# Kernel tuning notes

Hardware: AMD Instinct MI355X
Metric: run time of the kernel (lower is better)

Reference implementation:

```python
import jax, jax.numpy as jnp
import numpy as np

N_NODES = 100000
N_EDGES = 1600000
IN_CH = 64
OUT_CH = 64
EDGE_DIM = 32


def setup_inputs() -> dict:
    key = jax.random.key(0)
    ks = jax.random.split(key, 8)
    cat_dim = 2 * IN_CH + EDGE_DIM  # 160
    x = jax.random.normal(ks[0], (N_NODES, IN_CH), dtype=jnp.float32)
    edge_index = jax.random.randint(ks[1], (2, N_EDGES), 0, N_NODES, dtype=jnp.int64)
    edge_attr = jax.random.normal(ks[2], (N_EDGES, EDGE_DIM), dtype=jnp.float32)
    # linear1: (2*in + edge_dim) -> out ; stored as [in, out] for x @ W
    W1 = jax.random.normal(ks[3], (cat_dim, OUT_CH), dtype=jnp.float32) / np.sqrt(cat_dim)
    b1 = jnp.zeros((OUT_CH,), dtype=jnp.float32)
    gamma = jnp.ones((OUT_CH,), dtype=jnp.float32)
    beta = jnp.zeros((OUT_CH,), dtype=jnp.float32)
    W2 = jax.random.normal(ks[4], (OUT_CH, OUT_CH), dtype=jnp.float32) / np.sqrt(OUT_CH)
    b2 = jnp.zeros((OUT_CH,), dtype=jnp.float32)
    return {"x": x, "edge_index": edge_index, "edge_attr": edge_attr,
            "W1": W1, "b1": b1, "gamma": gamma, "beta": beta, "W2": W2, "b2": b2}


def _layer_norm(h, gamma, beta, eps=1e-5):
    mu = jnp.mean(h, axis=-1, keepdims=True)
    var = jnp.var(h, axis=-1, keepdims=True)
    return (h - mu) * jax.lax.rsqrt(var + eps) * gamma + beta


def reference(x, edge_index, edge_attr, W1, b1, gamma, beta, W2, b2):
    i, j = edge_index[0], edge_index[1]
    # gather source/target node features and concat with edge features: [E, 2*in+edge_dim]
    feats = jnp.concatenate([x[i], x[j], edge_attr], axis=-1)
    h = feats @ W1 + b1                       # [E, out]
    h = jax.nn.gelu(_layer_norm(h, gamma, beta), approximate=False)
    m = h @ W2 + b2                           # [E, out]
    # scatter-add messages onto target nodes j, dim_size = N
    return jax.ops.segment_sum(m, j, num_segments=x.shape[0])
```

## Files before the change

kernel.cpp:

```cpp
#include <hip/hip_runtime.h>
#include <math.h>


using short8 = __attribute__((ext_vector_type(8))) short;
using f32x4  = __attribute__((ext_vector_type(4))) float;

#define LDH 72

static __device__ __forceinline__ short f2bf(float f) {
    unsigned u = __float_as_uint(f);
    u += 0x7FFFu + ((u >> 16) & 1u);
    return (short)(u >> 16);
}

static __device__ __forceinline__ short8 pack8(float4 a, float4 b) {
    short8 r;
    r[0] = f2bf(a.x); r[1] = f2bf(a.y); r[2] = f2bf(a.z); r[3] = f2bf(a.w);
    r[4] = f2bf(b.x); r[5] = f2bf(b.y); r[6] = f2bf(b.z); r[7] = f2bf(b.w);
    return r;
}

__global__ __launch_bounds__(256) void prep_all(
    const float* __restrict__ x,
    const float* __restrict__ W1,
    const float* __restrict__ W2,
    short* __restrict__ Wt1,
    short* __restrict__ Wt2,
    short* __restrict__ xbf,
    float* __restrict__ out,
    int N, int out_elems, int doX)
{
    const int tid = blockIdx.x * 256 + threadIdx.x;
    const int TT  = gridDim.x * 256;

    const int nf4 = out_elems >> 2;
    const float4 z = make_float4(0.f, 0.f, 0.f, 0.f);
    for (int i = tid; i < nf4; i += TT) ((float4*)out)[i] = z;
    for (int i = (nf4 << 2) + tid; i < out_elems; i += TT) out[i] = 0.f;

    for (int t = tid; t < 160 * 64; t += TT) {
        int k = t / 64, n = t % 64;
        Wt1[n * 160 + k] = f2bf(W1[t]);
    }
    for (int t = tid; t < 64 * 64; t += TT) {
        int k = t / 64, n = t % 64;
        Wt2[n * 64 + k] = f2bf(W2[t]);
    }
    if (doX) {
        const float4* xf4 = (const float4*)x;
        for (int t = tid; t < N * 8; t += TT) {
            float4 a = xf4[2 * t];
            float4 b = xf4[2 * t + 1];
            ((short8*)xbf)[t] = pack8(a, b);
        }
    }
}

template <bool XBF>
__global__ __launch_bounds__(256) void mpconv_mfma(
    const float* __restrict__ x,
    const short* __restrict__ xbf,
    const int*   __restrict__ ei,
    const float* __restrict__ ea,
    const short* __restrict__ Wt1,
    const float* __restrict__ b1,
    const float* __restrict__ gam,
    const float* __restrict__ bet,
    const short* __restrict__ Wt2,
    const float* __restrict__ b2,
    float*       __restrict__ out,
    int E)
{
    __shared__ __align__(16) short Hlds[4][64][LDH];

    const int wave = threadIdx.x >> 6;
    const int lane = threadIdx.x & 63;
    const int g    = lane >> 4;
    const int col  = lane & 15;
    const int eb   = blockIdx.x * 256 + wave * 64;

    int aedge[4], ii[4], jj[4];
#pragma unroll
    for (int mt = 0; mt < 4; mt++) {
        int e = eb + mt * 16 + col;
        e = (e < E) ? e : (E - 1);
        aedge[mt] = e;
        ii[mt] = ei[e];
        jj[mt] = ei[E + e];
    }

    float b1c[4], gc[4], bc[4], b2c[4];
#pragma unroll
    for (int nt = 0; nt < 4; nt++) {
        int c = col + 16 * nt;
        b1c[nt] = b1[c]; gc[nt] = gam[c]; bc[nt] = bet[c]; b2c[nt] = b2[c];
    }

    f32x4 acc[4][4];
#pragma unroll
    for (int mt = 0; mt < 4; mt++)
#pragma unroll
        for (int nt = 0; nt < 4; nt++)
            acc[mt][nt] = (f32x4){0.f, 0.f, 0.f, 0.f};

#pragma unroll
    for (int ks = 0; ks < 5; ks++) {
        const int k0 = ks * 32;
        const int kk = k0 + g * 8;

        short8 afrag[4];
#pragma unroll
        for (int mt = 0; mt < 4; mt++) {
            if (XBF && k0 < 64) {
                afrag[mt] = *(const short8*)(xbf + (size_t)ii[mt] * 64 + kk);
            } else if (XBF && k0 < 128) {
                afrag[mt] = *(const short8*)(xbf + (size_t)jj[mt] * 64 + (kk - 64));
            } else {
                const float* s;
                if (k0 < 64)       s = x  + (size_t)ii[mt] * 64 + kk;
                else if (k0 < 128) s = x  + (size_t)jj[mt] * 64 + (kk - 64);
                else               s = ea + (size_t)aedge[mt] * 32 + (kk - 128);
                float4 a = *(const float4*)s;
                float4 b = *(const float4*)(s + 4);
                afrag[mt] = pack8(a, b);
            }
        }
        short8 bfrag[4];
#pragma unroll
        for (int nt = 0; nt < 4; nt++)
            bfrag[nt] = *(const short8*)(Wt1 + (size_t)(col + 16 * nt) * 160 + kk);

#pragma unroll
        for (int mt = 0; mt < 4; mt++)
#pragma unroll
            for (int nt = 0; nt < 4; nt++)
                acc[mt][nt] = __builtin_amdgcn_mfma_f32_16x16x32_bf16(
                    afrag[mt], bfrag[nt], acc[mt][nt], 0, 0, 0);
    }

#pragma unroll
    for (int mt = 0; mt < 4; mt++) {
        float s[4] = {0.f, 0.f, 0.f, 0.f};
        float q[4] = {0.f, 0.f, 0.f, 0.f};
#pragma unroll
        for (int nt = 0; nt < 4; nt++) {
#pragma unroll
            for (int r = 0; r < 4; r++) {
                float v = acc[mt][nt][r] + b1c[nt];
                acc[mt][nt][r] = v;
                s[r] += v;
                q[r] += v * v;
            }
        }
#pragma unroll
        for (int m = 1; m < 16; m <<= 1) {
#pragma unroll
            for (int r = 0; r < 4; r++) {
                s[r] += __shfl_xor(s[r], m);
                q[r] += __shfl_xor(q[r], m);
            }
        }
#pragma unroll
        for (int r = 0; r < 4; r++) {
            float mu  = s[r] * (1.0f / 64.0f);
            float var = q[r] * (1.0f / 64.0f) - mu * mu;
            float inv = rsqrtf(var + 1e-5f);
            int row = mt * 16 + g * 4 + r;
#pragma unroll
            for (int nt = 0; nt < 4; nt++) {
                float h = (acc[mt][nt][r] - mu) * inv * gc[nt] + bc[nt];
                h = 0.5f * h * (1.0f + erff(h * 0.70710678118654752f));
                Hlds[wave][row][col + 16 * nt] = f2bf(h);
            }
        }
    }
    __syncthreads();

    f32x4 acc2[4][4];
#pragma unroll
    for (int mt = 0; mt < 4; mt++)
#pragma unroll
        for (int nt = 0; nt < 4; nt++)
            acc2[mt][nt] = (f32x4){0.f, 0.f, 0.f, 0.f};

#pragma unroll
    for (int ks = 0; ks < 2; ks++) {
        const int kk = ks * 32 + g * 8;
        short8 af[4], bf[4];
#pragma unroll
        for (int mt = 0; mt < 4; mt++)
            af[mt] = *(const short8*)&Hlds[wave][mt * 16 + col][kk];
#pragma unroll
        for (int nt = 0; nt < 4; nt++)
            bf[nt] = *(const short8*)(Wt2 + (size_t)(col + 16 * nt) * 64 + kk);
#pragma unroll
        for (int mt = 0; mt < 4; mt++)
#pragma unroll
            for (int nt = 0; nt < 4; nt++)
                acc2[mt][nt] = __builtin_amdgcn_mfma_f32_16x16x32_bf16(
                    af[mt], bf[nt], acc2[mt][nt], 0, 0, 0);
    }

#pragma unroll
    for (int mt = 0; mt < 4; mt++) {
#pragma unroll
        for (int r = 0; r < 4; r++) {
            int e = eb + mt * 16 + g * 4 + r;
            if (e < E) {
                int dst = ei[E + e];
                float* op = out + (size_t)dst * 64 + col;
#pragma unroll
                for (int nt = 0; nt < 4; nt++)
                    unsafeAtomicAdd(op + 16 * nt, acc2[mt][nt][r] + b2c[nt]);
            }
        }
    }
}

extern "C" void kernel_launch(void* const* d_in, const int* in_sizes, int n_in,
                              void* d_out, int out_size, void* d_ws, size_t ws_size,
                              hipStream_t stream)
{
    const float* x   = (const float*)d_in[0];
    const int*   ei  = (const int*)  d_in[1];
    const float* ea  = (const float*)d_in[2];
    const float* W1  = (const float*)d_in[3];
    const float* b1  = (const float*)d_in[4];
    const float* gam = (const float*)d_in[5];
    const float* bet = (const float*)d_in[6];
    const float* W2  = (const float*)d_in[7];
    const float* b2  = (const float*)d_in[8];
    float* out = (float*)d_out;

    const int E = in_sizes[1] / 2;
    const int N = in_sizes[0] / 64;

    short* Wt1 = (short*)d_ws;
    short* Wt2 = Wt1 + 160 * 64;
    const size_t woff = (size_t)(160 * 64 + 64 * 64) * sizeof(short);
    short* xbf = (short*)((char*)d_ws + woff);
    const size_t need_xbf = woff + (size_t)N * 64 * sizeof(short);
    const int use_xbf = (ws_size >= need_xbf) ? 1 : 0;

    hipLaunchKernelGGL(prep_all, dim3(1024), dim3(256), 0, stream,
                       x, W1, W2, Wt1, Wt2, xbf, out, N, out_size, use_xbf);

    {
        int grid = (E + 255) / 256;
        if (use_xbf)
            hipLaunchKernelGGL(mpconv_mfma<true>, dim3(grid), dim3(256), 0, stream,
                               x, xbf, ei, ea, Wt1, b1, gam, bet, Wt2, b2, out, E);
        else
            hipLaunchKernelGGL(mpconv_mfma<false>, dim3(grid), dim3(256), 0, stream,
                               x, xbf, ei, ea, Wt1, b1, gam, bet, Wt2, b2, out, E);
    }
}
```

Measured before the change: 692.9 us.

## Sort edges by destination and pre-reduce messages per wave before atomics

Adds a counting sort of edges by destination node: a histogram, a two-level scan and a scatter that builds an (edge, src, dst) index array. The fused edge kernel then walks the sorted edges, stages each 32-row slice of the output messages in shared memory and sums runs that share a destination before issuing one atomic per run. The goal is to cut global atomic traffic and improve locality of the scatter-add. In exchange it adds four small kernels and a 16-byte-per-edge array, and reads of edge_attr and x[i] become scattered.

```diff
diff --git a/kernel.cpp b/kernel.cpp
--- a/kernel.cpp
+++ b/kernel.cpp
@@ -6,6 +6,8 @@
 using f32x4  = __attribute__((ext_vector_type(4))) float;
 
 #define LDH 72
+#define WREG 9472
+#define SMEM_BYTES (4 * WREG)
 
 static __device__ __forceinline__ short f2bf(float f) {
     unsigned u = __float_as_uint(f);
@@ -27,8 +29,9 @@
     short* __restrict__ Wt1,
     short* __restrict__ Wt2,
     short* __restrict__ xbf,
+    int*   __restrict__ counts,
     float* __restrict__ out,
-    int N, int out_elems, int doX)
+    int N, int out_elems, int doX, int doSort)
 {
     const int tid = blockIdx.x * 256 + threadIdx.x;
     const int TT  = gridDim.x * 256;
@@ -37,6 +40,9 @@
     const float4 z = make_float4(0.f, 0.f, 0.f, 0.f);
     for (int i = tid; i < nf4; i += TT) ((float4*)out)[i] = z;
     for (int i = (nf4 << 2) + tid; i < out_elems; i += TT) out[i] = 0.f;
+
+    if (doSort)
+        for (int i = tid; i < N; i += TT) counts[i] = 0;
 
     for (int t = tid; t < 160 * 64; t += TT) {
         int k = t / 64, n = t % 64;
@@ -54,6 +60,239 @@
             ((short8*)xbf)[t] = pack8(a, b);
         }
     }
+}
+
+__global__ void hist_dst(const int* __restrict__ ei, int* __restrict__ counts, int E)
+{
+    int e = blockIdx.x * blockDim.x + threadIdx.x;
+    if (e < E) atomicAdd(&counts[ei[E + e]], 1);
+}
+
+__global__ __launch_bounds__(256) void scan_local(const int* __restrict__ counts,
+                                                  int* __restrict__ offs,
+                                                  int* __restrict__ bsum, int N)
+{
+    __shared__ int sc[256];
+    const int t = threadIdx.x;
+    const int i = blockIdx.x * 256 + t;
+    int v = (i < N) ? counts[i] : 0;
+    sc[t] = v;
+    __syncthreads();
+    for (int d = 1; d < 256; d <<= 1) {
+        int u = (t >= d) ? sc[t - d] : 0;
+        __syncthreads();
+        sc[t] += u;
+        __syncthreads();
+    }
+    if (i < N) offs[i] = sc[t] - v;
+    if (t == 255) bsum[blockIdx.x] = sc[255];
+}
+
+__global__ __launch_bounds__(1024) void scan_tops(const int* __restrict__ bsum,
+                                                  int* __restrict__ boff, int nb)
+{
+    __shared__ int sc[1024];
+    const int t = threadIdx.x;
+    int v = (t < nb) ? bsum[t] : 0;
+    sc[t] = v;
+    __syncthreads();
+    for (int d = 1; d < 1024; d <<= 1) {
+        int u = (t >= d) ? sc[t - d] : 0;
+        __syncthreads();
+        sc[t] += u;
+        __syncthreads();
+    }
+    if (t < nb) boff[t] = sc[t] - v;
+}
+
+__global__ void build_etri(const int* __restrict__ ei, int* __restrict__ offs,
+                           const int* __restrict__ boff,
+                           int4* __restrict__ etri, int E)
+{
+    int e = blockIdx.x * blockDim.x + threadIdx.x;
+    if (e < E) {
+        int src = ei[e];
+        int dst = ei[E + e];
+        int pos = atomicAdd(&offs[dst], 1) + boff[dst >> 8];
+        etri[pos] = make_int4(e, src, dst, 0);
+    }
+}
+
+__global__ __launch_bounds__(256) void mpconv_sorted(
+    const short* __restrict__ xbf,
+    const float* __restrict__ ea,
+    const short* __restrict__ Wt1,
+    const float* __restrict__ b1,
+    const float* __restrict__ gam,
+    const float* __restrict__ bet,
+    const short* __restrict__ Wt2,
+    const float* __restrict__ b2,
+    const int4*  __restrict__ etri,
+    float*       __restrict__ out,
+    int E)
+{
+    __shared__ __align__(16) char smem[SMEM_BYTES];
+
+    const int wave = threadIdx.x >> 6;
+    const int lane = threadIdx.x & 63;
+    const int g    = lane >> 4;
+    const int col  = lane & 15;
+    const int eb   = blockIdx.x * 256 + wave * 64;
+
+    char* wbase = smem + wave * WREG;
+    short (*Hl)[LDH] = (short (*)[LDH])wbase;
+    float (*Hf)[66]  = (float (*)[66])wbase;
+    int*  dstL       = (int*)(wbase + 9216);
+
+    int aedge[4], ii[4], jj[4];
+#pragma unroll
+    for (int mt = 0; mt < 4; mt++) {
+        int ep = eb + mt * 16 + col;
+        bool v = (ep < E);
+        int epc = v ? ep : (E - 1);
+        int4 t4 = etri[epc];
+        aedge[mt] = t4.x;
+        ii[mt] = t4.y;
+        jj[mt] = t4.z;
+        if (g == 0) dstL[mt * 16 + col] = v ? t4.z : -1;
+    }
+
+    float b1c[4], gc[4], bc[4], b2c[4];
+#pragma unroll
+    for (int nt = 0; nt < 4; nt++) {
+        int c = col + 16 * nt;
+        b1c[nt] = b1[c]; gc[nt] = gam[c]; bc[nt] = bet[c]; b2c[nt] = b2[c];
+    }
+
+    f32x4 acc[4][4];
+#pragma unroll
+    for (int mt = 0; mt < 4; mt++)
+#pragma unroll
+        for (int nt = 0; nt < 4; nt++)
+            acc[mt][nt] = (f32x4){0.f, 0.f, 0.f, 0.f};
+
+#pragma unroll
+    for (int ks = 0; ks < 5; ks++) {
+        const int k0 = ks * 32;
+        const int kk = k0 + g * 8;
+
+        short8 afrag[4];
+#pragma unroll
+        for (int mt = 0; mt < 4; mt++) {
+            if (k0 < 64) {
+                afrag[mt] = *(const short8*)(xbf + (size_t)ii[mt] * 64 + kk);
+            } else if (k0 < 128) {
+                afrag[mt] = *(const short8*)(xbf + (size_t)jj[mt] * 64 + (kk - 64));
+            } else {
+                const float* s = ea + (size_t)aedge[mt] * 32 + (kk - 128);
+                float4 a = *(const float4*)s;
+                float4 b = *(const float4*)(s + 4);
+                afrag[mt] = pack8(a, b);
+            }
+        }
+        short8 bfrag[4];
+#pragma unroll
+        for (int nt = 0; nt < 4; nt++)
+            bfrag[nt] = *(const short8*)(Wt1 + (size_t)(col + 16 * nt) * 160 + kk);
+
+#pragma unroll
+        for (int mt = 0; mt < 4; mt++)
+#pragma unroll
+            for (int nt = 0; nt < 4; nt++)
+                acc[mt][nt] = __builtin_amdgcn_mfma_f32_16x16x32_bf16(
+                    afrag[mt], bfrag[nt], acc[mt][nt], 0, 0, 0);
+    }
+
+#pragma unroll
+    for (int mt = 0; mt < 4; mt++) {
+        float s[4] = {0.f, 0.f, 0.f, 0.f};
+        float q[4] = {0.f, 0.f, 0.f, 0.f};
+#pragma unroll
+        for (int nt = 0; nt < 4; nt++) {
+#pragma unroll
+            for (int r = 0; r < 4; r++) {
+                float v = acc[mt][nt][r] + b1c[nt];
+                acc[mt][nt][r] = v;
+                s[r] += v;
+                q[r] += v * v;
+            }
+        }
+#pragma unroll
+        for (int m = 1; m < 16; m <<= 1) {
+#pragma unroll
+            for (int r = 0; r < 4; r++) {
+                s[r] += __shfl_xor(s[r], m);
+                q[r] += __shfl_xor(q[r], m);
+            }
+        }
+#pragma unroll
+        for (int r = 0; r < 4; r++) {
+            float mu  = s[r] * (1.0f / 64.0f);
+            float var = q[r] * (1.0f / 64.0f) - mu * mu;
+            float inv = rsqrtf(var + 1e-5f);
+            int row = mt * 16 + g * 4 + r;
+#pragma unroll
+            for (int nt = 0; nt < 4; nt++) {
+                float h = (acc[mt][nt][r] - mu) * inv * gc[nt] + bc[nt];
+                h = 0.5f * h * (1.0f + erff(h * 0.70710678118654752f));
+                Hl[row][col + 16 * nt] = f2bf(h);
+            }
+        }
+    }
+
+    f32x4 acc2[4][4];
+#pragma unroll
+    for (int mt = 0; mt < 4; mt++)
+#pragma unroll
+        for (int nt = 0; nt < 4; nt++)
+            acc2[mt][nt] = (f32x4){0.f, 0.f, 0.f, 0.f};
+
+#pragma unroll
+    for (int ks = 0; ks < 2; ks++) {
+        const int kk = ks * 32 + g * 8;
+        short8 af[4], bf[4];
+#pragma unroll
+        for (int mt = 0; mt < 4; mt++)
+            af[mt] = *(const short8*)&Hl[mt * 16 + col][kk];
+#pragma unroll
+        for (int nt = 0; nt < 4; nt++)
+            bf[nt] = *(const short8*)(Wt2 + (size_t)(col + 16 * nt) * 64 + kk);
+#pragma unroll
+        for (int mt = 0; mt < 4; mt++)
+#pragma unroll
+            for (int nt = 0; nt < 4; nt++)
+                acc2[mt][nt] = __builtin_amdgcn_mfma_f32_16x16x32_bf16(
+                    af[mt], bf[nt], acc2[mt][nt], 0, 0, 0);
+    }
+
+    int cur = -1;
+    float sum = 0.f;
+#pragma unroll
+    for (int p = 0; p < 2; p++) {
+#pragma unroll
+        for (int m2 = 0; m2 < 2; m2++) {
+            int mt = 2 * p + m2;
+#pragma unroll
+            for (int nt = 0; nt < 4; nt++)
+#pragma unroll
+                for (int r = 0; r < 4; r++)
+                    Hf[m2 * 16 + g * 4 + r][col + 16 * nt] =
+                        acc2[mt][nt][r] + b2c[nt];
+        }
+#pragma unroll 4
+        for (int row = 0; row < 32; row++) {
+            int d = dstL[p * 32 + row];
+            float v = Hf[row][lane];
+            if (d != cur) {
+                if (cur >= 0)
+                    unsafeAtomicAdd(out + (size_t)cur * 64 + lane, sum);
+                cur = d; sum = 0.f;
+            }
+            if (d >= 0) sum += v;
+        }
+    }
+    if (cur >= 0)
+        unsafeAtomicAdd(out + (size_t)cur * 64 + lane, sum);
 }
 
 template <bool XBF>
@@ -234,24 +473,48 @@
 
     const int E = in_sizes[1] / 2;
     const int N = in_sizes[0] / 64;
+    const int nb = (N + 255) / 256;
 
     short* Wt1 = (short*)d_ws;
     short* Wt2 = Wt1 + 160 * 64;
     const size_t woff = (size_t)(160 * 64 + 64 * 64) * sizeof(short);
     short* xbf = (short*)((char*)d_ws + woff);
     const size_t need_xbf = woff + (size_t)N * 64 * sizeof(short);
-    const int use_xbf = (ws_size >= need_xbf) ? 1 : 0;
-
-    hipLaunchKernelGGL(prep_all, dim3(1024), dim3(256), 0, stream,
-                       x, W1, W2, Wt1, Wt2, xbf, out, N, out_size, use_xbf);
-
-    {
-        int grid = (E + 255) / 256;
+    const size_t soff = (need_xbf + 255) & ~(size_t)255;
+    int* counts = (int*)((char*)d_ws + soff);
+    int* offs   = counts + N;
+    int* bsum   = offs + N;
+    int* boff   = bsum + 1024;
+    const size_t eoff = (soff + (size_t)N * 8 + 8192 + 255) & ~(size_t)255;
+    int4* etri  = (int4*)((char*)d_ws + eoff);
+    const size_t need_full = eoff + (size_t)E * sizeof(int4);
+
+    const int use_xbf  = (ws_size >= need_xbf) ? 1 : 0;
+    const int use_sort = (ws_size >= need_full && nb <= 1024 && use_xbf) ? 1 : 0;
+
+    hipLaunchKernelGGL(prep_all, dim3(2048), dim3(256), 0, stream,
+                       x, W1, W2, Wt1, Wt2, xbf, counts, out,
+                       N, out_size, use_xbf, use_sort);
+
+    if (use_sort) {
+        const int gridE = (E + 255) / 256;
+        hipLaunchKernelGGL(hist_dst, dim3(gridE), dim3(256), 0, stream,
+                           ei, counts, E);
+        hipLaunchKernelGGL(scan_local, dim3(nb), dim3(256), 0, stream,
+                           counts, offs, bsum, N);
+        hipLaunchKernelGGL(scan_tops, dim3(1), dim3(1024), 0, stream,
+                           bsum, boff, nb);
+        hipLaunchKernelGGL(build_etri, dim3(gridE), dim3(256), 0, stream,
+                           ei, offs, boff, etri, E);
+        hipLaunchKernelGGL(mpconv_sorted, dim3(gridE), dim3(256), 0, stream,
+                           xbf, ea, Wt1, b1, gam, bet, Wt2, b2, etri, out, E);
+    } else {
+        const int gridE = (E + 255) / 256;
         if (use_xbf)
-            hipLaunchKernelGGL(mpconv_mfma<true>, dim3(grid), dim3(256), 0, stream,
+            hipLaunchKernelGGL(mpconv_mfma<true>, dim3(gridE), dim3(256), 0, stream,
                                x, xbf, ei, ea, Wt1, b1, gam, bet, Wt2, b2, out, E);
         else
-            hipLaunchKernelGGL(mpconv_mfma<false>, dim3(grid), dim3(256), 0, stream,
+            hipLaunchKernelGGL(mpconv_mfma<false>, dim3(gridE), dim3(256), 0, stream,
                                x, xbf, ei, ea, Wt1, b1, gam, bet, Wt2, b2, out, E);
     }
 }
```

Measured after the change: 741.7 us. 7.0% more time.
